# Kernel optimization log

Hardware: AMD Instinct MI355X
Metric: run time of the kernel (lower is better)

## Reference

```python
import jax, jax.numpy as jnp
import numpy as np

# matcher cost weights (init_kwargs)
W_CLASS, W_3DCENTER, W_BBOX, W_GIOU = 2.0, 10.0, 5.0, 2.0
ALPHA, GAMMA, EPS = 0.25, 2.0, 1e-8


def _box_cxcylrtb_to_xyxy(b):
    # (cx, cy, l, r, t, b) -> (x1, y1, x2, y2)
    cx, cy, l, r, t, bo = (b[..., i] for i in range(6))
    return jnp.stack([cx - l, cy - t, cx + r, cy + bo], axis=-1)


def _generalized_box_iou(b1, b2):
    # b1 [N,4], b2 [M,4] in xyxy -> GIoU matrix [N,M]
    area1 = (b1[:, 2] - b1[:, 0]) * (b1[:, 3] - b1[:, 1])
    area2 = (b2[:, 2] - b2[:, 0]) * (b2[:, 3] - b2[:, 1])
    lt = jnp.maximum(b1[:, None, :2], b2[None, :, :2])
    rb = jnp.minimum(b1[:, None, 2:], b2[None, :, 2:])
    wh = jnp.clip(rb - lt, 0.0)
    inter = wh[..., 0] * wh[..., 1]
    union = area1[:, None] + area2[None, :] - inter
    iou = inter / union
    lt_e = jnp.minimum(b1[:, None, :2], b2[None, :, :2])
    rb_e = jnp.maximum(b1[:, None, 2:], b2[None, :, 2:])
    wh_e = jnp.clip(rb_e - lt_e, 0.0)
    area_e = wh_e[..., 0] * wh_e[..., 1]
    return iou - (area_e - union) / area_e


def _l1_cdist(a, b):
    return jnp.abs(a[:, None, :] - b[None, :, :]).sum(-1)


def _cost_matrix(pred_logits, pred_boxes, tgt_labels, tgt_boxes):
    bs, nq, _ = pred_boxes.shape
    out_prob = jax.nn.sigmoid(pred_logits.reshape(bs * nq, -1))
    tgt_ids = tgt_labels.reshape(-1)
    neg = (1.0 - ALPHA) * out_prob ** GAMMA * -jnp.log(1.0 - out_prob + EPS)
    pos = ALPHA * (1.0 - out_prob) ** GAMMA * -jnp.log(out_prob + EPS)
    cost_class = (pos - neg)[:, tgt_ids]              # [bs*nq, bs*nt]
    out_flat = pred_boxes.reshape(bs * nq, 6)
    tgt_flat = tgt_boxes.reshape(-1, 6)
    cost_3dcenter = _l1_cdist(out_flat[:, 0:2], tgt_flat[:, 0:2])
    cost_bbox = _l1_cdist(out_flat[:, 2:6], tgt_flat[:, 2:6])
    cost_giou = -_generalized_box_iou(_box_cxcylrtb_to_xyxy(out_flat), _box_cxcylrtb_to_xyxy(tgt_flat))
    C = W_BBOX * cost_bbox + W_3DCENTER * cost_3dcenter + W_CLASS * cost_class + W_GIOU * cost_giou
    return C.reshape(bs, nq, -1)


def _lsa(cost):
    # Rectangular linear sum assignment (Jonker-Volgenant / e-maxx Hungarian),
    # scipy.optimize.linear_sum_assignment compatible (row-sorted output).
    cost = np.asarray(cost, dtype=np.float64)
    transposed = cost.shape[0] > cost.shape[1]
    if transposed:
        cost = cost.T
    n, m = cost.shape  # n <= m
    u = np.zeros(n + 1)
    v = np.zeros(m + 1)
    p = np.zeros(m + 1, dtype=np.int64)    # p[j] = row matched to col j (1-indexed)
    way = np.zeros(m + 1, dtype=np.int64)
    INF = np.inf
    for i in range(1, n + 1):
        p[0] = i
        j0 = 0
        minv = np.full(m + 1, INF)
        used = np.zeros(m + 1, dtype=bool)
        while True:
            used[j0] = True
            i0 = p[j0]
            free = ~used[1:]
            cur = cost[i0 - 1, :] - u[i0] - v[1:]
            upd = free & (cur < minv[1:])
            minv[1:][upd] = cur[upd]
            way[1:][upd] = j0
            cand = np.where(free, minv[1:], INF)
            j1 = int(np.argmin(cand)) + 1
            delta = cand[j1 - 1]
            u[p[used]] += delta
            v[used] -= delta
            minv[~used] -= delta
            j0 = j1
            if p[j0] == 0:
                break
        while j0 != 0:
            j1 = way[j0]
            p[j0] = p[j1]
            j0 = j1
    cols = np.nonzero(p[1:])[0]
    rows = p[1:][cols] - 1
    if transposed:
        rows, cols = cols, rows
    order = np.argsort(rows)
    return rows[order], cols[order]


def _assign(Cn, nt, group_num):
    # per-sample block-diagonal cost slicing + per-group Hungarian, like the torch loop
    bs, nq, _ = Cn.shape
    g_nq = nq // group_num
    pred_idx, tgt_idx = [], []
    for b in range(bs):
        Cb = Cn[b, :, b * nt:(b + 1) * nt]
        rows, cols = [], []
        for g in range(group_num):
            r, c = _lsa(Cb[g * g_nq:(g + 1) * g_nq])
            rows.append(r + g * g_nq)
            cols.append(c)
        pred_idx.append(np.concatenate(rows))
        tgt_idx.append(np.concatenate(cols))
    return np.stack(pred_idx), np.stack(tgt_idx)


def setup_inputs() -> dict:
    key = jax.random.key(0)
    k1, k2, k3, k4 = jax.random.split(key, 4)
    bs, nq, nc, nt = 16, 550, 91, 48
    return {
        "pred_logits": jax.random.normal(k1, (bs, nq, nc), jnp.float32),
        "pred_boxes": jax.random.uniform(k2, (bs, nq, 6), jnp.float32),
        "tgt_labels": jax.random.randint(k3, (bs, nt), 0, nc),
        "tgt_boxes": jax.random.uniform(k4, (bs, nt, 6), jnp.float32),
        "group_num": 11,
    }


def reference(pred_logits, pred_boxes, tgt_labels, tgt_boxes, group_num):
    C = _cost_matrix(pred_logits, pred_boxes, tgt_labels, tgt_boxes)  # [bs, nq, bs*nt]
    nt = tgt_boxes.shape[1]
    Cn = np.asarray(jax.device_get(C), dtype=np.float64)
    pi, ti = _assign(Cn, nt, int(group_num))
    return C, jnp.asarray(pi), jnp.asarray(ti)
```

## Files before the change

### kernel.cpp

```cpp
#include <hip/hip_runtime.h>
#include <math.h>

#define BS 16
#define NQ 550
#define NC 91
#define NT 48
#define GN 11
#define GQ 50
#define NTOT (BS * NT)
#define NROW 48
#define MCOL 50
#define NPAIR (GN * NT)
#define NLSA (BS * GN)

__device__ __forceinline__ float sigmoid_f32(float x) {
    double e = exp(-(double)x);
    return (float)(1.0 / (1.0 + e));
}
__device__ __forceinline__ float log_f32(float x) {
    return (float)log((double)x);
}
__device__ __forceinline__ float focal_cost(float x) {
    float prob = sigmoid_f32(x);
    float q = __fsub_rn(1.0f, prob);
    const float EPSF = 1e-8f;
    float lneg = log_f32(__fadd_rn(q, EPSF));
    float lpos = log_f32(__fadd_rn(prob, EPSF));
    float p2 = __fmul_rn(prob, prob);
    float q2 = __fmul_rn(q, q);
    float neg = __fmul_rn(__fmul_rn(0.75f, p2), -lneg);
    float pos = __fmul_rn(__fmul_rn(0.25f, q2), -lpos);
    return __fsub_rn(pos, neg);
}

__global__ __launch_bounds__(256) void focal_table_kernel(
    const float* __restrict__ logits, float* __restrict__ tab) {
    int idx = blockIdx.x * 256 + threadIdx.x;
    if (idx >= BS * NQ * NC) return;
    tab[idx] = focal_cost(logits[idx]);
}

template <bool USE_TAB>
__device__ __forceinline__ float cost_element(
    const float* __restrict__ tab, const float* __restrict__ logits,
    const float* __restrict__ pboxes, const int* __restrict__ labels,
    const float* __restrict__ tboxes, int p, int t)
{
    const float* pb = pboxes + (long)p * 6;
    float pcx = pb[0], pcy = pb[1], pl = pb[2], pr = pb[3], ptt = pb[4], pbo = pb[5];
    const float* tb = tboxes + (long)t * 6;
    float tcx = tb[0], tcy = tb[1], tl = tb[2], tr = tb[3], ttt = tb[4], tbo = tb[5];

    float c3d = __fadd_rn(fabsf(__fsub_rn(pcx, tcx)), fabsf(__fsub_rn(pcy, tcy)));
    float cbb = __fadd_rn(
                  __fadd_rn(
                    __fadd_rn(fabsf(__fsub_rn(pl, tl)), fabsf(__fsub_rn(pr, tr))),
                    fabsf(__fsub_rn(ptt, ttt))),
                  fabsf(__fsub_rn(pbo, tbo)));

    float px1 = __fsub_rn(pcx, pl), py1 = __fsub_rn(pcy, ptt);
    float px2 = __fadd_rn(pcx, pr), py2 = __fadd_rn(pcy, pbo);
    float tx1 = __fsub_rn(tcx, tl), ty1 = __fsub_rn(tcy, ttt);
    float tx2 = __fadd_rn(tcx, tr), ty2 = __fadd_rn(tcy, tbo);

    float area1 = __fmul_rn(__fsub_rn(px2, px1), __fsub_rn(py2, py1));
    float area2 = __fmul_rn(__fsub_rn(tx2, tx1), __fsub_rn(ty2, ty1));
    float ltx = fmaxf(px1, tx1), lty = fmaxf(py1, ty1);
    float rbx = fminf(px2, tx2), rby = fminf(py2, ty2);
    float wx = fmaxf(__fsub_rn(rbx, ltx), 0.0f);
    float wy = fmaxf(__fsub_rn(rby, lty), 0.0f);
    float inter = __fmul_rn(wx, wy);
    float uni = __fsub_rn(__fadd_rn(area1, area2), inter);
    float iou = __fdiv_rn(inter, uni);
    float ex1 = fminf(px1, tx1), ey1 = fminf(py1, ty1);
    float ex2 = fmaxf(px2, tx2), ey2 = fmaxf(py2, ty2);
    float ew = fmaxf(__fsub_rn(ex2, ex1), 0.0f);
    float eh = fmaxf(__fsub_rn(ey2, ey1), 0.0f);
    float earea = __fmul_rn(ew, eh);
    float giou = __fsub_rn(iou, __fdiv_rn(__fsub_rn(earea, uni), earea));
    float cgiou = -giou;

    int c = labels[t];
    float cclass;
    if (USE_TAB) cclass = tab[(long)p * NC + c];
    else         cclass = focal_cost(logits[(long)p * NC + c]);

    float out = __fmul_rn(5.0f, cbb);
    out = __fadd_rn(out, __fmul_rn(10.0f, c3d));
    out = __fadd_rn(out, __fmul_rn(2.0f, cclass));
    out = __fadd_rn(out, __fmul_rn(2.0f, cgiou));
    return out;
}

__device__ __forceinline__ double readlane_f64(double x, int l) {
    long long b = __double_as_longlong(x);
    int lo = __builtin_amdgcn_readlane((int)(b & 0xffffffffLL), l);
    int hi = __builtin_amdgcn_readlane((int)(b >> 32), l);
    return __longlong_as_double(((long long)hi << 32) | (unsigned int)lo);
}

template <int CTRL, int RM>
__device__ __forceinline__ double dpp_min_f64(double x) {
    long long b = __double_as_longlong(x);
    int lo = (int)(b & 0xffffffffLL);
    int hi = (int)(b >> 32);
    int tlo = __builtin_amdgcn_update_dpp(lo, lo, CTRL, RM, 0xf, false);
    int thi = __builtin_amdgcn_update_dpp(hi, hi, CTRL, RM, 0xf, false);
    double t = __longlong_as_double(((long long)thi << 32) | (unsigned int)tlo);
    return fmin(x, t);
}

__device__ __forceinline__ double wave_min_f64(double val) {
    double r = val;
    r = dpp_min_f64<0x111, 0xf>(r);
    r = dpp_min_f64<0x112, 0xf>(r);
    r = dpp_min_f64<0x114, 0xf>(r);
    r = dpp_min_f64<0x118, 0xf>(r);
    r = dpp_min_f64<0x142, 0xa>(r);
    r = dpp_min_f64<0x143, 0xc>(r);
    return readlane_f64(r, 63);
}

template <bool USE_TAB>
__global__ __launch_bounds__(256) void mega_kernel(
    const float* __restrict__ tab,
    const float* __restrict__ logits,
    const float* __restrict__ pboxes,
    const int*   __restrict__ labels,
    const float* __restrict__ tboxes,
    float*       __restrict__ C,
    float*       __restrict__ pi,
    float*       __restrict__ ti)
{
    if (blockIdx.x >= NLSA) {
        long idx = (long)(blockIdx.x - NLSA) * 256 + threadIdx.x;
        if (idx >= (long)BS * NQ * NTOT) return;
        int t = (int)(idx % NTOT);
        int p = (int)(idx / NTOT);
        C[idx] = cost_element<USE_TAB>(tab, logits, pboxes, labels, tboxes, p, t);
        return;
    }

    const int blk = blockIdx.x;
    const int b = blk / GN, g = blk % GN;
    const int tid = threadIdx.x;

    __shared__ double lcost[NROW * MCOL];

    for (int k = tid; k < NROW * MCOL; k += 256) {
        int i = k % NROW, j = k / NROW;
        float cf = cost_element<USE_TAB>(tab, logits, pboxes, labels, tboxes,
                                         b * NQ + g * GQ + j, b * NT + i);
        lcost[i * MCOL + j] = (double)cf;
    }
    __syncthreads();
    if (tid >= 64) return;

    const int lane = tid;
    const bool incol = (lane >= 1 && lane <= MCOL);
    const int cidx = incol ? lane - 1 : 0;
    const double INF = __builtin_inf();

    int    pcol_l = 0;
    double urow_l = 0.0;
    double v_l    = 0.0;
    int    way_l  = 0;
    double minv_l = INF;
    bool   used_l = false;

    for (int i = 1; i <= NROW; ++i) {
        if (lane == 0) { pcol_l = i; urow_l = 0.0; }
        minv_l = INF;
        used_l = false;
        int j0 = 0;
        int i0 = i;
        double u_i0 = 0.0;

        for (int guard = 0; guard <= MCOL + 1; ++guard) {
            used_l = used_l || (lane == j0);

            double cd  = lcost[(i0 - 1) * MCOL + cidx];
            bool freel = incol && !used_l;
            double cur = (cd - u_i0) - v_l;
            bool upd   = freel && (cur < minv_l);
            minv_l = upd ? cur : minv_l;
            way_l  = upd ? j0  : way_l;

            double val   = freel ? minv_l : INF;
            double delta = wave_min_f64(val);
            unsigned long long mm = __ballot(freel && (minv_l == delta));
            int j1 = (int)__builtin_ctzll(mm);

            urow_l = used_l ? urow_l + delta : urow_l;
            v_l    = used_l ? v_l - delta    : v_l;
            minv_l = freel  ? minv_l - delta : minv_l;

            int i0n = __builtin_amdgcn_readlane(pcol_l, j1);
            j0 = j1;
            if (i0n == 0) break;
            i0   = i0n;
            u_i0 = readlane_f64(urow_l, j1);
        }

        int j = j0;
        while (j != 0) {
            int wj    = __builtin_amdgcn_readlane(way_l, j);
            int pr    = __builtin_amdgcn_readlane(pcol_l, wj);
            double ur = readlane_f64(urow_l, wj);
            if (lane == j) { pcol_l = pr; urow_l = ur; }
            j = wj;
        }
    }

    unsigned long long asg = __ballot(incol && pcol_l != 0);
    if (incol && pcol_l != 0) {
        int k = __popcll(asg & ((1ull << lane) - 1));
        float* pib = pi + ((long)b * NPAIR + (long)g * NT);
        float* tib = ti + ((long)b * NPAIR + (long)g * NT);
        pib[k] = (float)(g * GQ + cidx);
        tib[k] = (float)(pcol_l - 1);
    }
}

extern "C" void kernel_launch(void* const* d_in, const int* in_sizes, int n_in,
                              void* d_out, int out_size, void* d_ws, size_t ws_size,
                              hipStream_t stream) {
    const float* logits = (const float*)d_in[0];
    const float* pboxes = (const float*)d_in[1];
    const int*   labels = (const int*)d_in[2];
    const float* tboxes = (const float*)d_in[3];

    float* out = (float*)d_out;
    float* C  = out;
    float* pi = out + (long)BS * NQ * NTOT;
    float* ti = pi + (long)BS * NPAIR;

    long total = (long)BS * NQ * NTOT;
    int cost_blocks = (int)((total + 255) / 256);
    int mega_blocks = NLSA + cost_blocks;

    const size_t tab_bytes = (size_t)BS * NQ * NC * sizeof(float);
    if (ws_size >= tab_bytes) {
        float* tab = (float*)d_ws;
        int tblocks = (BS * NQ * NC + 255) / 256;
        focal_table_kernel<<<tblocks, 256, 0, stream>>>(logits, tab);
        mega_kernel<true><<<mega_blocks, 256, 0, stream>>>(
            tab, logits, pboxes, labels, tboxes, C, pi, ti);
    } else {
        mega_kernel<false><<<mega_blocks, 256, 0, stream>>>(
            nullptr, logits, pboxes, labels, tboxes, C, pi, ti);
    }
}
```

Baseline: 191.7 us.

## Compute focal cost inline in fast fp32 and cache LSA cost column in registers

Removes the separate focal-table kernel and instead evaluates the focal class cost inline with fast fp32 exp/log intrinsics, replacing the double-precision exp/log. The LSA blocks now keep their cost tile in float with a padded shared layout, and each lane loads its 48-entry column into a register vector once, so the Hungarian inner loop avoids shared-memory reads. This saves one kernel launch, the table round-trip, and costly fp64 transcendentals. The trade-offs are reduced numerical accuracy, which may change the C values or the assignment results, and higher register pressure from the 48-element vector with a dynamic index.

```diff
diff --git a/kernel.cpp b/kernel.cpp
--- a/kernel.cpp
+++ b/kernel.cpp
@@ -12,37 +12,20 @@
 #define MCOL 50
 #define NPAIR (GN * NT)
 #define NLSA (BS * GN)
-
-__device__ __forceinline__ float sigmoid_f32(float x) {
-    double e = exp(-(double)x);
-    return (float)(1.0 / (1.0 + e));
-}
-__device__ __forceinline__ float log_f32(float x) {
-    return (float)log((double)x);
-}
-__device__ __forceinline__ float focal_cost(float x) {
-    float prob = sigmoid_f32(x);
-    float q = __fsub_rn(1.0f, prob);
-    const float EPSF = 1e-8f;
-    float lneg = log_f32(__fadd_rn(q, EPSF));
-    float lpos = log_f32(__fadd_rn(prob, EPSF));
-    float p2 = __fmul_rn(prob, prob);
-    float q2 = __fmul_rn(q, q);
-    float neg = __fmul_rn(__fmul_rn(0.75f, p2), -lneg);
-    float pos = __fmul_rn(__fmul_rn(0.25f, q2), -lpos);
-    return __fsub_rn(pos, neg);
-}
-
-__global__ __launch_bounds__(256) void focal_table_kernel(
-    const float* __restrict__ logits, float* __restrict__ tab) {
-    int idx = blockIdx.x * 256 + threadIdx.x;
-    if (idx >= BS * NQ * NC) return;
-    tab[idx] = focal_cost(logits[idx]);
-}
-
-template <bool USE_TAB>
+#define LPAD 51
+
+__device__ __forceinline__ float focal_cost_f32(float x) {
+    float prob = 1.0f / (1.0f + __expf(-x));
+    float q = 1.0f - prob;
+    float lneg = __logf(q + 1e-8f);
+    float lpos = __logf(prob + 1e-8f);
+    float neg = 0.75f * (prob * prob) * (-lneg);
+    float pos = 0.25f * (q * q) * (-lpos);
+    return pos - neg;
+}
+
 __device__ __forceinline__ float cost_element(
-    const float* __restrict__ tab, const float* __restrict__ logits,
+    const float* __restrict__ logits,
     const float* __restrict__ pboxes, const int* __restrict__ labels,
     const float* __restrict__ tboxes, int p, int t)
 {
@@ -80,10 +63,7 @@
     float giou = __fsub_rn(iou, __fdiv_rn(__fsub_rn(earea, uni), earea));
     float cgiou = -giou;
 
-    int c = labels[t];
-    float cclass;
-    if (USE_TAB) cclass = tab[(long)p * NC + c];
-    else         cclass = focal_cost(logits[(long)p * NC + c]);
+    float cclass = focal_cost_f32(logits[(long)p * NC + labels[t]]);
 
     float out = __fmul_rn(5.0f, cbb);
     out = __fadd_rn(out, __fmul_rn(10.0f, c3d));
@@ -121,9 +101,9 @@
     return readlane_f64(r, 63);
 }
 
-template <bool USE_TAB>
+typedef float fvec48 __attribute__((ext_vector_type(NROW)));
+
 __global__ __launch_bounds__(256) void mega_kernel(
-    const float* __restrict__ tab,
     const float* __restrict__ logits,
     const float* __restrict__ pboxes,
     const int*   __restrict__ labels,
@@ -137,7 +117,7 @@
         if (idx >= (long)BS * NQ * NTOT) return;
         int t = (int)(idx % NTOT);
         int p = (int)(idx / NTOT);
-        C[idx] = cost_element<USE_TAB>(tab, logits, pboxes, labels, tboxes, p, t);
+        C[idx] = cost_element(logits, pboxes, labels, tboxes, p, t);
         return;
     }
 
@@ -145,13 +125,12 @@
     const int b = blk / GN, g = blk % GN;
     const int tid = threadIdx.x;
 
-    __shared__ double lcost[NROW * MCOL];
+    __shared__ float lcostf[NROW * LPAD];
 
     for (int k = tid; k < NROW * MCOL; k += 256) {
         int i = k % NROW, j = k / NROW;
-        float cf = cost_element<USE_TAB>(tab, logits, pboxes, labels, tboxes,
-                                         b * NQ + g * GQ + j, b * NT + i);
-        lcost[i * MCOL + j] = (double)cf;
+        lcostf[i * LPAD + j] = cost_element(logits, pboxes, labels, tboxes,
+                                            b * NQ + g * GQ + j, b * NT + i);
     }
     __syncthreads();
     if (tid >= 64) return;
@@ -160,6 +139,10 @@
     const bool incol = (lane >= 1 && lane <= MCOL);
     const int cidx = incol ? lane - 1 : 0;
     const double INF = __builtin_inf();
+
+    fvec48 cv;
+#pragma unroll
+    for (int i = 0; i < NROW; ++i) cv[i] = lcostf[i * LPAD + cidx];
 
     int    pcol_l = 0;
     double urow_l = 0.0;
@@ -179,7 +162,8 @@
         for (int guard = 0; guard <= MCOL + 1; ++guard) {
             used_l = used_l || (lane == j0);
 
-            double cd  = lcost[(i0 - 1) * MCOL + cidx];
+            float cf = cv[i0 - 1];
+            double cd = (double)cf;
             bool freel = incol && !used_l;
             double cur = (cd - u_i0) - v_l;
             bool upd   = freel && (cur < minv_l);
@@ -239,15 +223,6 @@
     int cost_blocks = (int)((total + 255) / 256);
     int mega_blocks = NLSA + cost_blocks;
 
-    const size_t tab_bytes = (size_t)BS * NQ * NC * sizeof(float);
-    if (ws_size >= tab_bytes) {
-        float* tab = (float*)d_ws;
-        int tblocks = (BS * NQ * NC + 255) / 256;
-        focal_table_kernel<<<tblocks, 256, 0, stream>>>(logits, tab);
-        mega_kernel<true><<<mega_blocks, 256, 0, stream>>>(
-            tab, logits, pboxes, labels, tboxes, C, pi, ti);
-    } else {
-        mega_kernel<false><<<mega_blocks, 256, 0, stream>>>(
-            nullptr, logits, pboxes, labels, tboxes, C, pi, ti);
-    }
-}
+    mega_kernel<<<mega_blocks, 256, 0, stream>>>(
+        logits, pboxes, labels, tboxes, C, pi, ti);
+}
```

Result: slower. 354.2 us (+84.8%).
